# Kernel optimization log

Measured on AMD Instinct MI355X. Metric: run time of the kernel, lower is better.

The kernel has to match this reference:

```python
import jax, jax.numpy as jnp
import numpy as np

F = 256

def setup_inputs() -> dict:
    key = jax.random.key(0)
    ks = jax.random.split(key, 6)
    s = 1.0 / np.sqrt(F)
    x = jax.random.normal(ks[0], (16, 1024, F), dtype=jnp.float32)
    W_alpha = jax.random.uniform(ks[1], (F, F), minval=-s, maxval=s, dtype=jnp.float32)
    W_beta = jax.random.uniform(ks[2], (F, F), minval=-s, maxval=s, dtype=jnp.float32)
    W_unary = jax.random.uniform(ks[3], (F, F), minval=-s, maxval=s, dtype=jnp.float32)
    b_unary = jax.random.uniform(ks[4], (F,), minval=-s, maxval=s, dtype=jnp.float32)
    W_r = jax.random.uniform(ks[5], (F, F), minval=-s, maxval=s, dtype=jnp.float32)
    return {"x": x, "W_alpha": W_alpha, "W_beta": W_beta, "W_unary": W_unary, "b_unary": b_unary, "W_r": W_r}

def reference(x, W_alpha, W_beta, W_unary, b_unary, W_r):
    # x: [B, N, F]; torch Linear computes x @ W^T (+ b)
    B, N, _ = x.shape
    alpha = jnp.einsum('bnf,gf->bng', x, W_alpha)
    beta = jnp.einsum('bnf,gf->bng', x, W_beta)
    unary = jnp.einsum('bnf,gf->bng', x, W_unary) + b_unary
    # scores: alpha_i . beta_j, diagonal excluded (i == j skipped in loop)
    scores = jnp.einsum('bif,bjf->bij', alpha, beta)
    scores = scores * (1.0 - jnp.eye(N, dtype=x.dtype))
    att = jnp.einsum('bij,bjf->bif', scores, unary) / N
    out = jnp.einsum('bif,gf->big', att, W_r) + x
    return out
```

## Files before the change

### kernel.cpp

```cpp
#include <hip/hip_runtime.h>


typedef __bf16 bf16;
typedef float floatx4 __attribute__((ext_vector_type(4)));
typedef bf16 bf16x8 __attribute__((ext_vector_type(8)));

constexpr int FD = 256;
constexpr int NB = 16;
constexpr int NN = 1024;
constexpr int RR = NB * NN;

__device__ __forceinline__ bf16x8 cvt8(float4 a, float4 b) {
    bf16x8 o = { (bf16)a.x, (bf16)a.y, (bf16)a.z, (bf16)a.w,
                 (bf16)b.x, (bf16)b.y, (bf16)b.z, (bf16)b.w };
    return o;
}

__device__ __forceinline__ int pk(int r, int k) {
    return ((r >> 4) * 8 + (k >> 5)) * 512 + (((k >> 3) & 3) * 16 + (r & 15)) * 8 + (k & 7);
}

__global__ __launch_bounds__(256)
void prep(const float* __restrict__ Wa, const float* __restrict__ Wb,
          const float* __restrict__ Wu, const float* __restrict__ bu,
          const float* __restrict__ Wr,
          bf16* __restrict__ WfC, bf16* __restrict__ WfA, float* __restrict__ bc)
{
    const int blk = blockIdx.x, tid = threadIdx.x;
    if (blk < 256) {
        const int j = blk;
        float acc = 0.0f;
        for (int g = 0; g < FD; g += 4) {
            float4 wr = *(const float4*)&Wr[j * FD + g];
            acc += wr.x * Wu[g * FD + tid] + wr.y * Wu[(g + 1) * FD + tid]
                 + wr.z * Wu[(g + 2) * FD + tid] + wr.w * Wu[(g + 3) * FD + tid];
        }
        WfC[pk(j, tid)] = (bf16)acc;
    } else if (blk == 256) {
        float s = 0.0f;
        for (int g = 0; g < FD; g++) s += Wr[tid * FD + g] * bu[g];
        bc[tid] = s;
    } else {
        const int f = blk - 257;
        float acc = 0.0f;
        for (int k = 0; k < FD; k += 4) {
            acc += Wa[k * FD + f] * Wb[k * FD + tid]
                 + Wa[(k + 1) * FD + f] * Wb[(k + 1) * FD + tid]
                 + Wa[(k + 2) * FD + f] * Wb[(k + 2) * FD + tid]
                 + Wa[(k + 3) * FD + f] * Wb[(k + 3) * FD + tid];
        }
        WfA[pk(f, tid)] = (bf16)acc;
    }
}

__global__ __launch_bounds__(256, 4)
void proj(const float* __restrict__ x,
          const bf16* __restrict__ WfA, const bf16* __restrict__ WfC,
          bf16* __restrict__ abTp, bf16* __restrict__ U2Tp,
          const float* __restrict__ bc, float* __restrict__ dvec)
{
    __shared__ __align__(16) bf16 TrT[256 * 24];
    __shared__ float dsum[4][16];

    const int tid = threadIdx.x;
    const int wave = tid >> 6, lane = tid & 63;
    const int q = lane >> 4, l16 = lane & 15;
    const int bm = blockIdx.x * 16;
    const int b = bm >> 10, n0 = bm & (NN - 1);

    const float* xr = x + (size_t)(bm + l16) * FD;
    bf16x8 af[8];
    #pragma unroll
    for (int ks = 0; ks < 8; ks++) {
        const float* p = xr + ks * 32 + q * 8;
        af[ks] = cvt8(*(const float4*)p, *(const float4*)(p + 4));
    }

    floatx4 acc[2][4] = {};
    #pragma unroll
    for (int nj = 0; nj < 4; nj++) {
        const bf16* pA = WfA + (size_t)((wave * 4 + nj) * 8) * 512 + lane * 8;
        const bf16* pC = WfC + (size_t)((wave * 4 + nj) * 8) * 512 + lane * 8;
        #pragma unroll
        for (int ks = 0; ks < 8; ks++) {
            bf16x8 b0 = *(const bf16x8*)(pA + ks * 512);
            bf16x8 b1 = *(const bf16x8*)(pC + ks * 512);
            acc[0][nj] = __builtin_amdgcn_mfma_f32_16x16x32_bf16(af[ks], b0, acc[0][nj], 0, 0, 0);
            acc[1][nj] = __builtin_amdgcn_mfma_f32_16x16x32_bf16(af[ks], b1, acc[1][nj], 0, 0, 0);
        }
    }

    float pq[4];
    #pragma unroll
    for (int i = 0; i < 4; i++) {
        const int m = bm + q * 4 + i;
        float p = 0.0f;
        #pragma unroll
        for (int nj = 0; nj < 4; nj++)
            p += x[(size_t)m * FD + wave * 64 + nj * 16 + l16] * acc[0][nj][i];
        #pragma unroll
        for (int off = 1; off < 16; off <<= 1) p += __shfl_xor(p, off);
        pq[i] = p;
    }
    if (l16 == 0) {
        #pragma unroll
        for (int i = 0; i < 4; i++) dsum[wave][q * 4 + i] = pq[i];
    }
    __syncthreads();
    if (tid < 16) dvec[bm + tid] = dsum[0][tid] + dsum[1][tid] + dsum[2][tid] + dsum[3][tid];

    float bcv[4];
    #pragma unroll
    for (int nj = 0; nj < 4; nj++) bcv[nj] = bc[wave * 64 + nj * 16 + l16];

    const int o0 = (n0 >> 3) & 3;
    #pragma unroll
    for (int pass = 0; pass < 2; pass++) {
        __syncthreads();
        #pragma unroll
        for (int nj = 0; nj < 4; nj++)
            #pragma unroll
            for (int i = 0; i < 4; i++) {
                float v = acc[pass][nj][i];
                if (pass == 1) v += bcv[nj];
                TrT[(wave * 64 + nj * 16 + l16) * 24 + q * 4 + i] = (bf16)v;
            }
        __syncthreads();
        bf16* dst = (pass ? U2Tp : abTp) + (size_t)b * FD * NN;
        #pragma unroll
        for (int it = 0; it < 2; it++) {
            int c = tid + it * 256;
            int r = c >> 1, h = c & 1;
            bf16x8 v = *(const bf16x8*)&TrT[r * 24 + h * 8];
            int chunk = (r >> 4) * 32 + (n0 >> 5);
            *(bf16x8*)&dst[(size_t)chunk * 512 + ((o0 + h) * 16 + (r & 15)) * 8] = v;
        }
    }
}

__global__ __launch_bounds__(256, 2)
void m2_mfma(const bf16* __restrict__ U2Tp, const bf16* __restrict__ abTp, bf16* __restrict__ Gp)
{
    __shared__ __align__(16) bf16 Tr[64][40];
    const int lin = blockIdx.x;
    const int xcd = lin & 7, loc = lin >> 3;
    const int b = xcd + 8 * (loc >> 5);
    const int tile = loc & 31;
    const int bj = (tile >> 3) * 64, bk = (tile & 7) * 32;

    const int tid = threadIdx.x;
    const int wave = tid >> 6, lane = tid & 63;
    const int q = lane >> 4, l16 = lane & 15;

    const bf16* Ab = U2Tp + (size_t)b * FD * NN + lane * 8;
    const bf16* Bb = abTp + (size_t)b * FD * NN + lane * 8;
    const int ach = ((bj >> 4) + wave) * 32;
    const int bch0 = (bk >> 4) * 32;
    const int bch1 = ((bk >> 4) + 1) * 32;

    floatx4 acc[2] = {};
    #pragma unroll 8
    for (int n5 = 0; n5 < 32; n5++) {
        bf16x8 af = *(const bf16x8*)&Ab[(size_t)(ach + n5) * 512];
        bf16x8 b0 = *(const bf16x8*)&Bb[(size_t)(bch0 + n5) * 512];
        bf16x8 b1 = *(const bf16x8*)&Bb[(size_t)(bch1 + n5) * 512];
        acc[0] = __builtin_amdgcn_mfma_f32_16x16x32_bf16(af, b0, acc[0], 0, 0, 0);
        acc[1] = __builtin_amdgcn_mfma_f32_16x16x32_bf16(af, b1, acc[1], 0, 0, 0);
    }

    #pragma unroll
    for (int i = 0; i < 4; i++)
        #pragma unroll
        for (int kj = 0; kj < 2; kj++)
            Tr[wave * 16 + q * 4 + i][kj * 16 + l16] = (bf16)acc[kj][i];
    __syncthreads();
    {
        const int jj = tid >> 2, oct = tid & 3;
        bf16x8 v = *(const bf16x8*)&Tr[jj][oct * 8];
        const int chunk = ((bj + jj) >> 4) * 8 + (bk >> 5);
        *(bf16x8*)&Gp[(size_t)b * FD * FD + (size_t)chunk * 512
                      + (oct * 16 + ((bj + jj) & 15)) * 8] = v;
    }
}

__global__ __launch_bounds__(256, 4)
void final_mfma(const float* __restrict__ x, const bf16* __restrict__ Gp,
                const float* __restrict__ dvec, const bf16* __restrict__ WfC,
                const float* __restrict__ bc, float* __restrict__ out)
{
    const int tid = threadIdx.x;
    const int wave = tid >> 6, lane = tid & 63;
    const int q = lane >> 4, l16 = lane & 15;
    const int bn = blockIdx.x * 64, bm = blockIdx.y * 64;
    const int b = bm >> 10;

    const float* xr = x + (size_t)(bm + wave * 16 + l16) * FD;
    const bf16* Gb = Gp + (size_t)b * FD * FD + lane * 8;
    const bf16* Wc = WfC + lane * 8;
    const int cb = bn >> 4;

    floatx4 acc[4] = {}, acc2[4] = {};
    #pragma unroll
    for (int ks = 0; ks < 8; ks++) {
        const int ko = ks * 32 + q * 8;
        bf16x8 af = cvt8(*(const float4*)&xr[ko], *(const float4*)&xr[ko + 4]);
        #pragma unroll
        for (int nj = 0; nj < 4; nj++) {
            bf16x8 bg = *(const bf16x8*)&Gb[(size_t)((cb + nj) * 8 + ks) * 512];
            bf16x8 bu = *(const bf16x8*)&Wc[(size_t)((cb + nj) * 8 + ks) * 512];
            acc[nj]  = __builtin_amdgcn_mfma_f32_16x16x32_bf16(af, bg, acc[nj], 0, 0, 0);
            acc2[nj] = __builtin_amdgcn_mfma_f32_16x16x32_bf16(af, bu, acc2[nj], 0, 0, 0);
        }
    }

    float bcv[4];
    #pragma unroll
    for (int nj = 0; nj < 4; nj++) bcv[nj] = bc[bn + nj * 16 + l16];

    #pragma unroll
    for (int i = 0; i < 4; i++) {
        const int m = bm + wave * 16 + q * 4 + i;
        const float d = dvec[m];
        #pragma unroll
        for (int nj = 0; nj < 4; nj++) {
            const int n = bn + nj * 16 + l16;
            const float u2 = acc2[nj][i] + bcv[nj];
            const float v = (acc[nj][i] - d * u2) * (1.0f / 1024.0f);
            out[(size_t)m * FD + n] = v + x[(size_t)m * FD + n];
        }
    }
}

extern "C" void kernel_launch(void* const* d_in, const int* in_sizes, int n_in,
                              void* d_out, int out_size, void* d_ws, size_t ws_size,
                              hipStream_t stream)
{
    const float* x  = (const float*)d_in[0];
    const float* Wa = (const float*)d_in[1];
    const float* Wb = (const float*)d_in[2];
    const float* Wu = (const float*)d_in[3];
    const float* bu = (const float*)d_in[4];
    const float* Wr = (const float*)d_in[5];
    float* out = (float*)d_out;

    char* w = (char*)d_ws;
    bf16* WfC   = (bf16*)w;  w += (size_t)FD * FD * 2;
    bf16* WfA   = (bf16*)w;  w += (size_t)FD * FD * 2;
    float* bc   = (float*)w; w += (size_t)FD * 4;
    bf16* abTp  = (bf16*)w;  w += (size_t)RR * FD * 2;
    bf16* U2Tp  = (bf16*)w;  w += (size_t)RR * FD * 2;
    bf16* Gp    = (bf16*)w;  w += (size_t)NB * FD * FD * 2;
    float* dvec = (float*)w; w += (size_t)RR * 4;

    dim3 blk(256);

    prep<<<dim3(513), blk, 0, stream>>>(Wa, Wb, Wu, bu, Wr, WfC, WfA, bc);

    proj<<<dim3(1024), blk, 0, stream>>>(x, WfA, WfC, abTp, U2Tp, bc, dvec);

    m2_mfma<<<dim3(512), blk, 0, stream>>>(U2Tp, abTp, Gp);

    final_mfma<<<dim3(4, 256), blk, 0, stream>>>(x, Gp, dvec, WfC, bc, out);
}
```

Baseline: 136.7 us.

## Fuse projection, Gram and output kernels into one persistent kernel with counters

Merges the proj, m2_mfma and final_mfma kernels into one 1024-block kernel. Per-batch atomic counters, reset in prep, let each stage start as soon as its batch's inputs are ready, instead of waiting at kernel boundaries. This removes two launch gaps and tail drains and lets stages from different batches overlap. It relies on all 1024 blocks being co-resident (4 per CU) to avoid deadlock, and the spin-waits plus extra shared memory may reduce occupancy.

Result: slower. 343.4 us (+151.3%).

```diff
diff --git a/kernel.cpp b/kernel.cpp
--- a/kernel.cpp
+++ b/kernel.cpp
@@ -24,7 +24,8 @@
 void prep(const float* __restrict__ Wa, const float* __restrict__ Wb,
           const float* __restrict__ Wu, const float* __restrict__ bu,
           const float* __restrict__ Wr,
-          bf16* __restrict__ WfC, bf16* __restrict__ WfA, float* __restrict__ bc)
+          bf16* __restrict__ WfC, bf16* __restrict__ WfA, float* __restrict__ bc,
+          int* __restrict__ cnt)
 {
     const int blk = blockIdx.x, tid = threadIdx.x;
     if (blk < 256) {
@@ -37,6 +38,7 @@
         }
         WfC[pk(j, tid)] = (bf16)acc;
     } else if (blk == 256) {
+        if (tid < 32) cnt[tid] = 0;
         float s = 0.0f;
         for (int g = 0; g < FD; g++) s += Wr[tid * FD + g] * bu[g];
         bc[tid] = s;
@@ -53,180 +55,195 @@
     }
 }
 
+__device__ __forceinline__ void wait_for(int* c, int target) {
+    if (threadIdx.x == 0) {
+        while (__hip_atomic_load(c, __ATOMIC_RELAXED, __HIP_MEMORY_SCOPE_AGENT) < target)
+            __builtin_amdgcn_s_sleep(16);
+        (void)__hip_atomic_load(c, __ATOMIC_ACQUIRE, __HIP_MEMORY_SCOPE_AGENT);
+    }
+    __syncthreads();
+}
+__device__ __forceinline__ void publish(int* c) {
+    __syncthreads();
+    if (threadIdx.x == 0) {
+        __threadfence();
+        __hip_atomic_fetch_add(c, 1, __ATOMIC_RELEASE, __HIP_MEMORY_SCOPE_AGENT);
+    }
+}
+
 __global__ __launch_bounds__(256, 4)
-void proj(const float* __restrict__ x,
-          const bf16* __restrict__ WfA, const bf16* __restrict__ WfC,
-          bf16* __restrict__ abTp, bf16* __restrict__ U2Tp,
-          const float* __restrict__ bc, float* __restrict__ dvec)
+void fused(const float* __restrict__ x,
+           const bf16* __restrict__ WfA, const bf16* __restrict__ WfC,
+           bf16* __restrict__ abTp, bf16* __restrict__ U2Tp, bf16* __restrict__ Gp,
+           const float* __restrict__ bc, float* __restrict__ dvec,
+           float* __restrict__ out, int* __restrict__ cnt)
 {
     __shared__ __align__(16) bf16 TrT[256 * 24];
     __shared__ float dsum[4][16];
-
+    __shared__ __align__(16) bf16 Tr[64][40];
+
+    int* cnt_p = cnt;
+    int* cnt_m = cnt + 16;
+
+    const int bid = blockIdx.x;
     const int tid = threadIdx.x;
     const int wave = tid >> 6, lane = tid & 63;
     const int q = lane >> 4, l16 = lane & 15;
-    const int bm = blockIdx.x * 16;
-    const int b = bm >> 10, n0 = bm & (NN - 1);
-
-    const float* xr = x + (size_t)(bm + l16) * FD;
-    bf16x8 af[8];
-    #pragma unroll
-    for (int ks = 0; ks < 8; ks++) {
-        const float* p = xr + ks * 32 + q * 8;
-        af[ks] = cvt8(*(const float4*)p, *(const float4*)(p + 4));
-    }
-
-    floatx4 acc[2][4] = {};
-    #pragma unroll
-    for (int nj = 0; nj < 4; nj++) {
-        const bf16* pA = WfA + (size_t)((wave * 4 + nj) * 8) * 512 + lane * 8;
-        const bf16* pC = WfC + (size_t)((wave * 4 + nj) * 8) * 512 + lane * 8;
+
+    {
+        const int bm = bid * 16;
+        const int b = bm >> 10, n0 = bm & (NN - 1);
+
+        const float* xr = x + (size_t)(bm + l16) * FD;
+        bf16x8 af[8];
         #pragma unroll
         for (int ks = 0; ks < 8; ks++) {
-            bf16x8 b0 = *(const bf16x8*)(pA + ks * 512);
-            bf16x8 b1 = *(const bf16x8*)(pC + ks * 512);
-            acc[0][nj] = __builtin_amdgcn_mfma_f32_16x16x32_bf16(af[ks], b0, acc[0][nj], 0, 0, 0);
-            acc[1][nj] = __builtin_amdgcn_mfma_f32_16x16x32_bf16(af[ks], b1, acc[1][nj], 0, 0, 0);
-        }
-    }
-
-    float pq[4];
-    #pragma unroll
-    for (int i = 0; i < 4; i++) {
-        const int m = bm + q * 4 + i;
-        float p = 0.0f;
-        #pragma unroll
-        for (int nj = 0; nj < 4; nj++)
-            p += x[(size_t)m * FD + wave * 64 + nj * 16 + l16] * acc[0][nj][i];
-        #pragma unroll
-        for (int off = 1; off < 16; off <<= 1) p += __shfl_xor(p, off);
-        pq[i] = p;
-    }
-    if (l16 == 0) {
-        #pragma unroll
-        for (int i = 0; i < 4; i++) dsum[wave][q * 4 + i] = pq[i];
-    }
-    __syncthreads();
-    if (tid < 16) dvec[bm + tid] = dsum[0][tid] + dsum[1][tid] + dsum[2][tid] + dsum[3][tid];
-
-    float bcv[4];
-    #pragma unroll
-    for (int nj = 0; nj < 4; nj++) bcv[nj] = bc[wave * 64 + nj * 16 + l16];
-
-    const int o0 = (n0 >> 3) & 3;
-    #pragma unroll
-    for (int pass = 0; pass < 2; pass++) {
+            const float* p = xr + ks * 32 + q * 8;
+            af[ks] = cvt8(*(const float4*)p, *(const float4*)(p + 4));
+        }
+
+        floatx4 acc[2][4] = {};
+        #pragma unroll
+        for (int nj = 0; nj < 4; nj++) {
+            const bf16* pA = WfA + (size_t)((wave * 4 + nj) * 8) * 512 + lane * 8;
+            const bf16* pC = WfC + (size_t)((wave * 4 + nj) * 8) * 512 + lane * 8;
+            #pragma unroll
+            for (int ks = 0; ks < 8; ks++) {
+                bf16x8 b0 = *(const bf16x8*)(pA + ks * 512);
+                bf16x8 b1 = *(const bf16x8*)(pC + ks * 512);
+                acc[0][nj] = __builtin_amdgcn_mfma_f32_16x16x32_bf16(af[ks], b0, acc[0][nj], 0, 0, 0);
+                acc[1][nj] = __builtin_amdgcn_mfma_f32_16x16x32_bf16(af[ks], b1, acc[1][nj], 0, 0, 0);
+            }
+        }
+
+        float pq[4];
+        #pragma unroll
+        for (int i = 0; i < 4; i++) {
+            const int m = bm + q * 4 + i;
+            float p = 0.0f;
+            #pragma unroll
+            for (int nj = 0; nj < 4; nj++)
+                p += x[(size_t)m * FD + wave * 64 + nj * 16 + l16] * acc[0][nj][i];
+            #pragma unroll
+            for (int off = 1; off < 16; off <<= 1) p += __shfl_xor(p, off);
+            pq[i] = p;
+        }
+        if (l16 == 0) {
+            #pragma unroll
+            for (int i = 0; i < 4; i++) dsum[wave][q * 4 + i] = pq[i];
+        }
         __syncthreads();
-        #pragma unroll
-        for (int nj = 0; nj < 4; nj++)
-            #pragma unroll
-            for (int i = 0; i < 4; i++) {
-                float v = acc[pass][nj][i];
-                if (pass == 1) v += bcv[nj];
-                TrT[(wave * 64 + nj * 16 + l16) * 24 + q * 4 + i] = (bf16)v;
-            }
+        if (tid < 16) dvec[bm + tid] = dsum[0][tid] + dsum[1][tid] + dsum[2][tid] + dsum[3][tid];
+
+        float bcv[4];
+        #pragma unroll
+        for (int nj = 0; nj < 4; nj++) bcv[nj] = bc[wave * 64 + nj * 16 + l16];
+
+        const int o0 = (n0 >> 3) & 3;
+        #pragma unroll
+        for (int pass = 0; pass < 2; pass++) {
+            __syncthreads();
+            #pragma unroll
+            for (int nj = 0; nj < 4; nj++)
+                #pragma unroll
+                for (int i = 0; i < 4; i++) {
+                    float v = acc[pass][nj][i];
+                    if (pass == 1) v += bcv[nj];
+                    TrT[(wave * 64 + nj * 16 + l16) * 24 + q * 4 + i] = (bf16)v;
+                }
+            __syncthreads();
+            bf16* dst = (pass ? U2Tp : abTp) + (size_t)b * FD * NN;
+            #pragma unroll
+            for (int it = 0; it < 2; it++) {
+                int c = tid + it * 256;
+                int r = c >> 1, h = c & 1;
+                bf16x8 v = *(const bf16x8*)&TrT[r * 24 + h * 8];
+                int chunk = (r >> 4) * 32 + (n0 >> 5);
+                *(bf16x8*)&dst[(size_t)chunk * 512 + ((o0 + h) * 16 + (r & 15)) * 8] = v;
+            }
+        }
+        publish(&cnt_p[b]);
+    }
+
+    if ((bid & 63) < 32) {
+        const int b = ((bid >> 6) + 15) & 15;
+        const int tile = bid & 31;
+        const int bj = (tile >> 3) * 64, bk = (tile & 7) * 32;
+
+        wait_for(&cnt_p[b], 64);
+
+        const bf16* Ab = U2Tp + (size_t)b * FD * NN + lane * 8;
+        const bf16* Bb = abTp + (size_t)b * FD * NN + lane * 8;
+        const int ach = ((bj >> 4) + wave) * 32;
+        const int bch0 = (bk >> 4) * 32;
+        const int bch1 = ((bk >> 4) + 1) * 32;
+
+        floatx4 acc[2] = {};
+        #pragma unroll 8
+        for (int n5 = 0; n5 < 32; n5++) {
+            bf16x8 af = *(const bf16x8*)&Ab[(size_t)(ach + n5) * 512];
+            bf16x8 b0 = *(const bf16x8*)&Bb[(size_t)(bch0 + n5) * 512];
+            bf16x8 b1 = *(const bf16x8*)&Bb[(size_t)(bch1 + n5) * 512];
+            acc[0] = __builtin_amdgcn_mfma_f32_16x16x32_bf16(af, b0, acc[0], 0, 0, 0);
+            acc[1] = __builtin_amdgcn_mfma_f32_16x16x32_bf16(af, b1, acc[1], 0, 0, 0);
+        }
+
+        #pragma unroll
+        for (int i = 0; i < 4; i++)
+            #pragma unroll
+            for (int kj = 0; kj < 2; kj++)
+                Tr[wave * 16 + q * 4 + i][kj * 16 + l16] = (bf16)acc[kj][i];
         __syncthreads();
-        bf16* dst = (pass ? U2Tp : abTp) + (size_t)b * FD * NN;
-        #pragma unroll
-        for (int it = 0; it < 2; it++) {
-            int c = tid + it * 256;
-            int r = c >> 1, h = c & 1;
-            bf16x8 v = *(const bf16x8*)&TrT[r * 24 + h * 8];
-            int chunk = (r >> 4) * 32 + (n0 >> 5);
-            *(bf16x8*)&dst[(size_t)chunk * 512 + ((o0 + h) * 16 + (r & 15)) * 8] = v;
-        }
-    }
-}
-
-__global__ __launch_bounds__(256, 2)
-void m2_mfma(const bf16* __restrict__ U2Tp, const bf16* __restrict__ abTp, bf16* __restrict__ Gp)
-{
-    __shared__ __align__(16) bf16 Tr[64][40];
-    const int lin = blockIdx.x;
-    const int xcd = lin & 7, loc = lin >> 3;
-    const int b = xcd + 8 * (loc >> 5);
-    const int tile = loc & 31;
-    const int bj = (tile >> 3) * 64, bk = (tile & 7) * 32;
-
-    const int tid = threadIdx.x;
-    const int wave = tid >> 6, lane = tid & 63;
-    const int q = lane >> 4, l16 = lane & 15;
-
-    const bf16* Ab = U2Tp + (size_t)b * FD * NN + lane * 8;
-    const bf16* Bb = abTp + (size_t)b * FD * NN + lane * 8;
-    const int ach = ((bj >> 4) + wave) * 32;
-    const int bch0 = (bk >> 4) * 32;
-    const int bch1 = ((bk >> 4) + 1) * 32;
-
-    floatx4 acc[2] = {};
-    #pragma unroll 8
-    for (int n5 = 0; n5 < 32; n5++) {
-        bf16x8 af = *(const bf16x8*)&Ab[(size_t)(ach + n5) * 512];
-        bf16x8 b0 = *(const bf16x8*)&Bb[(size_t)(bch0 + n5) * 512];
-        bf16x8 b1 = *(const bf16x8*)&Bb[(size_t)(bch1 + n5) * 512];
-        acc[0] = __builtin_amdgcn_mfma_f32_16x16x32_bf16(af, b0, acc[0], 0, 0, 0);
-        acc[1] = __builtin_amdgcn_mfma_f32_16x16x32_bf16(af, b1, acc[1], 0, 0, 0);
-    }
-
-    #pragma unroll
-    for (int i = 0; i < 4; i++)
-        #pragma unroll
-        for (int kj = 0; kj < 2; kj++)
-            Tr[wave * 16 + q * 4 + i][kj * 16 + l16] = (bf16)acc[kj][i];
-    __syncthreads();
+        {
+            const int jj = tid >> 2, oct = tid & 3;
+            bf16x8 v = *(const bf16x8*)&Tr[jj][oct * 8];
+            const int chunk = ((bj + jj) >> 4) * 8 + (bk >> 5);
+            *(bf16x8*)&Gp[(size_t)b * FD * FD + (size_t)chunk * 512
+                          + (oct * 16 + ((bj + jj) & 15)) * 8] = v;
+        }
+        publish(&cnt_m[b]);
+    }
+
     {
-        const int jj = tid >> 2, oct = tid & 3;
-        bf16x8 v = *(const bf16x8*)&Tr[jj][oct * 8];
-        const int chunk = ((bj + jj) >> 4) * 8 + (bk >> 5);
-        *(bf16x8*)&Gp[(size_t)b * FD * FD + (size_t)chunk * 512
-                      + (oct * 16 + ((bj + jj) & 15)) * 8] = v;
-    }
-}
-
-__global__ __launch_bounds__(256, 4)
-void final_mfma(const float* __restrict__ x, const bf16* __restrict__ Gp,
-                const float* __restrict__ dvec, const bf16* __restrict__ WfC,
-                const float* __restrict__ bc, float* __restrict__ out)
-{
-    const int tid = threadIdx.x;
-    const int wave = tid >> 6, lane = tid & 63;
-    const int q = lane >> 4, l16 = lane & 15;
-    const int bn = blockIdx.x * 64, bm = blockIdx.y * 64;
-    const int b = bm >> 10;
-
-    const float* xr = x + (size_t)(bm + wave * 16 + l16) * FD;
-    const bf16* Gb = Gp + (size_t)b * FD * FD + lane * 8;
-    const bf16* Wc = WfC + lane * 8;
-    const int cb = bn >> 4;
-
-    floatx4 acc[4] = {}, acc2[4] = {};
-    #pragma unroll
-    for (int ks = 0; ks < 8; ks++) {
-        const int ko = ks * 32 + q * 8;
-        bf16x8 af = cvt8(*(const float4*)&xr[ko], *(const float4*)&xr[ko + 4]);
-        #pragma unroll
-        for (int nj = 0; nj < 4; nj++) {
-            bf16x8 bg = *(const bf16x8*)&Gb[(size_t)((cb + nj) * 8 + ks) * 512];
-            bf16x8 bu = *(const bf16x8*)&Wc[(size_t)((cb + nj) * 8 + ks) * 512];
-            acc[nj]  = __builtin_amdgcn_mfma_f32_16x16x32_bf16(af, bg, acc[nj], 0, 0, 0);
-            acc2[nj] = __builtin_amdgcn_mfma_f32_16x16x32_bf16(af, bu, acc2[nj], 0, 0, 0);
-        }
-    }
-
-    float bcv[4];
-    #pragma unroll
-    for (int nj = 0; nj < 4; nj++) bcv[nj] = bc[bn + nj * 16 + l16];
-
-    #pragma unroll
-    for (int i = 0; i < 4; i++) {
-        const int m = bm + wave * 16 + q * 4 + i;
-        const float d = dvec[m];
-        #pragma unroll
-        for (int nj = 0; nj < 4; nj++) {
-            const int n = bn + nj * 16 + l16;
-            const float u2 = acc2[nj][i] + bcv[nj];
-            const float v = (acc[nj][i] - d * u2) * (1.0f / 1024.0f);
-            out[(size_t)m * FD + n] = v + x[(size_t)m * FD + n];
+        const int b = bid >> 6, t = bid & 63;
+        const int bm = b * NN + (t >> 2) * 64, bn = (t & 3) * 64;
+
+        wait_for(&cnt_m[b], 32);
+
+        const float* xr = x + (size_t)(bm + wave * 16 + l16) * FD;
+        const bf16* Gb = Gp + (size_t)b * FD * FD + lane * 8;
+        const bf16* Wc = WfC + lane * 8;
+        const int cb = bn >> 4;
+
+        floatx4 acc[4] = {}, acc2[4] = {};
+        #pragma unroll
+        for (int ks = 0; ks < 8; ks++) {
+            const int ko = ks * 32 + q * 8;
+            bf16x8 af = cvt8(*(const float4*)&xr[ko], *(const float4*)&xr[ko + 4]);
+            #pragma unroll
+            for (int nj = 0; nj < 4; nj++) {
+                bf16x8 bg = *(const bf16x8*)&Gb[(size_t)((cb + nj) * 8 + ks) * 512];
+                bf16x8 bu = *(const bf16x8*)&Wc[(size_t)((cb + nj) * 8 + ks) * 512];
+                acc[nj]  = __builtin_amdgcn_mfma_f32_16x16x32_bf16(af, bg, acc[nj], 0, 0, 0);
+                acc2[nj] = __builtin_amdgcn_mfma_f32_16x16x32_bf16(af, bu, acc2[nj], 0, 0, 0);
+            }
+        }
+
+        float bcv[4];
+        #pragma unroll
+        for (int nj = 0; nj < 4; nj++) bcv[nj] = bc[bn + nj * 16 + l16];
+
+        #pragma unroll
+        for (int i = 0; i < 4; i++) {
+            const int m = bm + wave * 16 + q * 4 + i;
+            const float d = dvec[m];
+            #pragma unroll
+            for (int nj = 0; nj < 4; nj++) {
+                const int n = bn + nj * 16 + l16;
+                const float u2 = acc2[nj][i] + bcv[nj];
+                const float v = (acc[nj][i] - d * u2) * (1.0f / 1024.0f);
+                out[(size_t)m * FD + n] = v + x[(size_t)m * FD + n];
+            }
         }
     }
 }
@@ -251,14 +268,11 @@
     bf16* U2Tp  = (bf16*)w;  w += (size_t)RR * FD * 2;
     bf16* Gp    = (bf16*)w;  w += (size_t)NB * FD * FD * 2;
     float* dvec = (float*)w; w += (size_t)RR * 4;
+    int* cnt    = (int*)w;   w += 256;
 
     dim3 blk(256);
 
-    prep<<<dim3(513), blk, 0, stream>>>(Wa, Wb, Wu, bu, Wr, WfC, WfA, bc);
-
-    proj<<<dim3(1024), blk, 0, stream>>>(x, WfA, WfC, abTp, U2Tp, bc, dvec);
-
-    m2_mfma<<<dim3(512), blk, 0, stream>>>(U2Tp, abTp, Gp);
-
-    final_mfma<<<dim3(4, 256), blk, 0, stream>>>(x, Gp, dvec, WfC, bc, out);
-}
+    prep<<<dim3(513), blk, 0, stream>>>(Wa, Wb, Wu, bu, Wr, WfC, WfA, bc, cnt);
+
+    fused<<<dim3(1024), blk, 0, stream>>>(x, WfA, WfC, abTp, U2Tp, Gp, bc, dvec, out, cnt);
+}
```
